# Kernel tuning notes

Measured on AMD Instinct MI355X. Metric: run time of the kernel, lower is better.

The kernel has to match this reference:

```python
import jax, jax.numpy as jnp
import numpy as np

N_NODES = 100000
N_EDGES = 1600000
IN_DIM = 300
HID = 128
N_CLASSES = 3
N_ASPECTS = 2048


def setup_inputs() -> dict:
    key = jax.random.key(0)
    ks = jax.random.split(key, 8)
    features = jax.random.normal(ks[0], (N_NODES, IN_DIM), dtype=jnp.float32)
    edge_index = jax.random.randint(ks[1], (2, N_EDGES), 0, N_NODES, dtype=jnp.int64)
    aspect_indices = jax.random.randint(ks[2], (N_ASPECTS,), 0, N_NODES, dtype=jnp.int64)
    W1 = jax.random.normal(ks[3], (IN_DIM, HID), dtype=jnp.float32) * (1.0 / np.sqrt(IN_DIM))
    b1 = jnp.zeros((HID,), dtype=jnp.float32)
    W2 = jax.random.normal(ks[4], (HID, HID), dtype=jnp.float32) * (1.0 / np.sqrt(HID))
    b2 = jnp.zeros((HID,), dtype=jnp.float32)
    Wc = jax.random.normal(ks[5], (HID, N_CLASSES), dtype=jnp.float32) * (1.0 / np.sqrt(HID))
    bc = jnp.zeros((N_CLASSES,), dtype=jnp.float32)
    return {"features": features, "edge_index": edge_index, "aspect_indices": aspect_indices,
            "W1": W1, "b1": b1, "W2": W2, "b2": b2, "Wc": Wc, "bc": bc}


def _gcn_norm(edge_index, num_nodes):
    # PyG GCNConv: add self-loops, symmetric normalization D^-1/2 (A+I) D^-1/2
    loop = jnp.arange(num_nodes, dtype=edge_index.dtype)
    src = jnp.concatenate([edge_index[0], loop])
    dst = jnp.concatenate([edge_index[1], loop])
    deg = jax.ops.segment_sum(jnp.ones_like(dst, dtype=jnp.float32), dst,
                              num_segments=num_nodes)
    deg_inv_sqrt = jnp.where(deg > 0, jax.lax.rsqrt(deg), 0.0)
    norm = deg_inv_sqrt[src] * deg_inv_sqrt[dst]  # [E + N]
    return src, dst, norm


def _gcn_conv(x, src, dst, norm, W, b, num_nodes):
    h = x @ W                            # transform first (dim reduction)
    msg = h[src] * norm[:, None]         # gather + scale  [E+N, HID]
    out = jax.ops.segment_sum(msg, dst, num_segments=num_nodes)  # scatter-add
    return out + b


def reference(features, edge_index, aspect_indices, W1, b1, W2, b2, Wc, bc):
    num_nodes = features.shape[0]
    src, dst, norm = _gcn_norm(edge_index, num_nodes)
    h = _gcn_conv(features, src, dst, norm, W1, b1, num_nodes)
    h = jax.nn.relu(h)
    # dropout(p=0.3) -> identity in eval mode
    h = _gcn_conv(h, src, dst, norm, W2, b2, num_nodes)
    aspect_embeddings = h[aspect_indices]          # [N_ASPECTS, HID]
    logits = aspect_embeddings @ Wc + bc           # [N_ASPECTS, 3]
    return logits
```

## Files before the change

kernel.cpp:

```cpp
#include <hip/hip_runtime.h>

constexpr int NN = 100000;
constexpr int NE = 1600000;
constexpr int IN_DIM = 300;
constexpr int HID = 128;
constexpr int NA = 2048;
constexpr int NF_CAP = 50000;
constexpr int G1_BLOCKS = 391;
constexpr int EDGE_BLOCKS = 782;

using short8 = __attribute__((ext_vector_type(8))) short;
using f32x4  = __attribute__((ext_vector_type(4))) float;

__device__ inline unsigned short f2bf(float x) {
    unsigned u = __float_as_uint(x);
    unsigned r = u + 0x7FFFu + ((u >> 16) & 1u);
    return (unsigned short)(r >> 16);
}
__device__ inline float bf2f(unsigned short h) {
    return __uint_as_float(((unsigned)h) << 16);
}

__device__ inline void gload_lds16(const void* g, void* l) {
    __builtin_amdgcn_global_load_lds(
        (const __attribute__((address_space(1))) unsigned int*)g,
        (__attribute__((address_space(3))) unsigned int*)l, 16, 0, 0);
}

__global__ void k_flag2(const int* __restrict__ asp, unsigned char* __restrict__ flags2,
                        int* __restrict__ flags1) {
    int i = blockIdx.x * blockDim.x + threadIdx.x;
    if (i < NA) {
        int n = asp[i];
        flags2[n] = 1;
        flags1[n] = 1;
    }
}

__global__ __launch_bounds__(1024) void k_scan2_local(const int* __restrict__ degi,
                                                      const int* __restrict__ flags1,
                                                      int* __restrict__ off,
                                                      int* __restrict__ off2,
                                                      int* __restrict__ blksum,
                                                      int* __restrict__ blksum2,
                                                      float* __restrict__ dis) {
    __shared__ int sh[1024];
    __shared__ int sh2[1024];
    int t = threadIdx.x;
    int base = blockIdx.x * 1024;
    int ok = (base + t < NN);
    int f = ok ? flags1[base + t] : 0;
    int d = ok ? degi[base + t] : 0;
    int v = f ? d : 0;
    if (ok) dis[base + t] = rsqrtf((float)d + 1.0f);
    sh[t] = v;
    sh2[t] = f;
    __syncthreads();
    for (int s = 1; s < 1024; s <<= 1) {
        int a = (t >= s) ? sh[t - s] : 0;
        int a2 = (t >= s) ? sh2[t - s] : 0;
        __syncthreads();
        sh[t] += a;
        sh2[t] += a2;
        __syncthreads();
    }
    if (ok) {
        off[base + t] = sh[t] - v;
        off2[base + t] = sh2[t] - f;
    }
    if (t == 1023) {
        blksum[blockIdx.x] = sh[1023];
        blksum2[blockIdx.x] = sh2[1023];
    }
}

__global__ __launch_bounds__(128) void k_scan2_blk(int* __restrict__ blksum,
                                                   int* __restrict__ blksum2, int nb) {
    __shared__ int sh[128];
    __shared__ int sh2[128];
    int t = threadIdx.x;
    int v = (t < nb) ? blksum[t] : 0;
    int v2 = (t < nb) ? blksum2[t] : 0;
    sh[t] = v;
    sh2[t] = v2;
    __syncthreads();
    for (int s = 1; s < 128; s <<= 1) {
        int a = (t >= s) ? sh[t - s] : 0;
        int a2 = (t >= s) ? sh2[t - s] : 0;
        __syncthreads();
        sh[t] += a;
        sh2[t] += a2;
        __syncthreads();
    }
    if (t < nb) {
        blksum[t] = sh[t] - v;
        blksum2[t] = sh2[t] - v2;
    }
}

__global__ void k_scan2_add(int* __restrict__ off, int* __restrict__ off2,
                            const int* __restrict__ blksum, const int* __restrict__ blksum2,
                            const int* __restrict__ flags1,
                            int* __restrict__ list, int* __restrict__ remap,
                            int* __restrict__ nf) {
    int i = blockIdx.x * blockDim.x + threadIdx.x;
    if (i < NN) {
        off[i] += blksum[i >> 10];
        int o2 = off2[i] + blksum2[i >> 10];
        off2[i] = o2;
        int f = flags1[i];
        if (f && o2 < NF_CAP) {
            list[o2] = i;
            remap[i] = o2;
        }
        if (i == NN - 1) {
            int tot = o2 + f;
            *nf = (tot < NF_CAP) ? tot : NF_CAP;
        }
    }
}

__global__ void k_prepB(const float* __restrict__ B, unsigned short* __restrict__ img,
                        int K, int NT) {
    int i = blockIdx.x * blockDim.x + threadIdx.x;
    if (i >= NT * 4096) return;
    int kt = i >> 12;
    int rem = i & 4095;
    int ct = rem >> 9;
    int s = rem & 511;
    int lg = s >> 7;
    int lr = (s >> 3) & 15;
    int j = s & 7;
    int k = kt * 32 + lg * 8 + j;
    int col = ct * 16 + lr;
    float v = (k < K) ? B[k * 128 + col] : 0.f;
    unsigned short hi = f2bf(v);
    unsigned short lo = f2bf(v - bf2f(hi));
    img[kt * 8192 + ct * 1024 + s] = hi;
    img[kt * 8192 + ct * 1024 + 512 + s] = lo;
}

template <int K, int NT>
__device__ __forceinline__ void gemm_dev(int gbid, const float* __restrict__ A,
        const unsigned short* __restrict__ Bimg,
        float* __restrict__ C, int M, const int* __restrict__ Mptr) {
    __shared__ alignas(16) unsigned short ldsB[2][8192];
    const int Mv = Mptr ? *Mptr : M;
    const int row0 = gbid * 128;
    if (row0 >= Mv) return;
    const int t = threadIdx.x;
    const int w = t >> 6;
    const int l = t & 63;
    const int lr = l & 15;
    const int lg = l >> 4;

    const int r0 = row0 + w * 16 + lr;
    const long a0 = (long)(r0 < Mv ? r0 : Mv - 1) * K + lg * 8;

    f32x4 acc[8];
#pragma unroll
    for (int ct = 0; ct < 8; ++ct) acc[ct] = (f32x4){0.f, 0.f, 0.f, 0.f};

    float4 A0[2], A1[2];

    auto LOADA = [&](float4* buf, int kt) {
        const int k0 = kt * 32 + lg * 8;
        const float* s0 = A + a0 + kt * 32;
        if (k0 + 8 <= K) {
            buf[0] = *(const float4*)(s0);
            buf[1] = *(const float4*)(s0 + 4);
        } else {
            float t0[8];
#pragma unroll
            for (int j = 0; j < 8; ++j) t0[j] = (k0 + j < K) ? s0[j] : 0.f;
            buf[0] = make_float4(t0[0], t0[1], t0[2], t0[3]);
            buf[1] = make_float4(t0[4], t0[5], t0[6], t0[7]);
        }
    };

    auto STAGE_B = [&](int buf, int kt) {
        const char* g = (const char*)Bimg + (long)kt * 16384 + w * 2048 + l * 16;
        gload_lds16(g, &ldsB[buf][w * 1024]);
        gload_lds16(g + 1024, &ldsB[buf][w * 1024 + 512]);
    };

    auto CONV = [&](const float4* buf, short8& h0, short8& e0) {
        float v0[8] = {buf[0].x, buf[0].y, buf[0].z, buf[0].w, buf[1].x, buf[1].y, buf[1].z, buf[1].w};
#pragma unroll
        for (int j = 0; j < 8; ++j) {
            unsigned short hi = f2bf(v0[j]);
            h0[j] = (short)hi;
            e0[j] = (short)f2bf(v0[j] - bf2f(hi));
        }
    };

    auto COMPUTE = [&](const unsigned short* bbuf, short8 ah, short8 al) {
#pragma unroll
        for (int ct = 0; ct < 8; ++ct) {
            const unsigned short* bp = bbuf + ct * 1024 + lg * 128 + lr * 8;
            short8 bh = *(const short8*)(bp);
            short8 bl = *(const short8*)(bp + 512);
            acc[ct] = __builtin_amdgcn_mfma_f32_16x16x32_bf16(ah, bh, acc[ct], 0, 0, 0);
            acc[ct] = __builtin_amdgcn_mfma_f32_16x16x32_bf16(al, bh, acc[ct], 0, 0, 0);
            acc[ct] = __builtin_amdgcn_mfma_f32_16x16x32_bf16(ah, bl, acc[ct], 0, 0, 0);
        }
    };

    LOADA(A0, 0);
    STAGE_B(0, 0);
    __syncthreads();
    for (int kt = 0; kt < NT; kt += 2) {
        if (kt + 1 < NT) {
            LOADA(A1, kt + 1);
            STAGE_B(1, kt + 1);
        }
        {
            short8 h0, e0;
            CONV(A0, h0, e0);
            COMPUTE(ldsB[0], h0, e0);
        }
        __syncthreads();
        if (kt + 1 < NT) {
            if (kt + 2 < NT) {
                LOADA(A0, kt + 2);
                STAGE_B(0, kt + 2);
            }
            short8 h0, e0;
            CONV(A1, h0, e0);
            COMPUTE(ldsB[1], h0, e0);
            __syncthreads();
        }
    }
#pragma unroll
    for (int ct = 0; ct < 8; ++ct)
#pragma unroll
        for (int r = 0; r < 4; ++r) {
            int row = row0 + w * 16 + lg * 4 + r;
            if (row < Mv) C[(long)row * 128 + ct * 16 + lr] = acc[ct][r];
        }
}

__global__ __launch_bounds__(512, 4) void k_fusedA(const float* __restrict__ A,
        const unsigned short* __restrict__ Bimg, float* __restrict__ C,
        const int* __restrict__ src, const int* __restrict__ dst,
        const unsigned char* __restrict__ flags2,
        int* __restrict__ degi, int* __restrict__ flags1) {
    if (blockIdx.x < G1_BLOCKS) {
        gemm_dev<IN_DIM, 10>(blockIdx.x, A, Bimg, C, NN, nullptr);
    } else {
        int e0 = (blockIdx.x - G1_BLOCKS) * 2048 + threadIdx.x * 4;
        if (e0 < NE) {
            int4 s4 = *(const int4*)(src + e0);
            int4 d4 = *(const int4*)(dst + e0);
            atomicAdd(&degi[d4.x], 1);
            atomicAdd(&degi[d4.y], 1);
            atomicAdd(&degi[d4.z], 1);
            atomicAdd(&degi[d4.w], 1);
            if (flags2[d4.x]) flags1[s4.x] = 1;
            if (flags2[d4.y]) flags1[s4.y] = 1;
            if (flags2[d4.z]) flags1[s4.z] = 1;
            if (flags2[d4.w]) flags1[s4.w] = 1;
        }
    }
}

__global__ __launch_bounds__(512, 4) void k_fusedB(const float* __restrict__ A,
        const unsigned short* __restrict__ Bimg, float* __restrict__ C,
        const int* __restrict__ src, const int* __restrict__ dst,
        const int* __restrict__ flags1,
        int* __restrict__ off, int* __restrict__ csr) {
    if (blockIdx.x < G1_BLOCKS) {
        gemm_dev<IN_DIM, 10>(blockIdx.x + G1_BLOCKS, A, Bimg, C, NN, nullptr);
    } else {
        int e0 = (blockIdx.x - G1_BLOCKS) * 2048 + threadIdx.x * 4;
        if (e0 < NE) {
            int4 s4 = *(const int4*)(src + e0);
            int4 d4 = *(const int4*)(dst + e0);
            if (flags1[d4.x]) csr[atomicAdd(&off[d4.x], 1)] = s4.x;
            if (flags1[d4.y]) csr[atomicAdd(&off[d4.y], 1)] = s4.y;
            if (flags1[d4.z]) csr[atomicAdd(&off[d4.z], 1)] = s4.z;
            if (flags1[d4.w]) csr[atomicAdd(&off[d4.w], 1)] = s4.w;
        }
    }
}

__global__ __launch_bounds__(512, 4) void k_gemm2(const float* __restrict__ A,
        const unsigned short* __restrict__ Bimg, float* __restrict__ C,
        const int* __restrict__ nf) {
    gemm_dev<HID, 4>(blockIdx.x, A, Bimg, C, 0, nf);
}

__global__ __launch_bounds__(256) void k_gather1(const int* __restrict__ list,
                                                 const int* __restrict__ nf,
                                                 const int* __restrict__ csr,
                                                 const int* __restrict__ offpost,
                                                 const float* __restrict__ dis,
                                                 const float* __restrict__ h1,
                                                 const float* __restrict__ b1,
                                                 float* __restrict__ out) {
    int wave = threadIdx.x >> 6;
    int lane = threadIdx.x & 63;
    int half = lane >> 5;
    int sl = lane & 31;
    int idx = blockIdx.x * 4 + wave;
    if (idx >= *nf) return;
    int n = list[idx];
    int start = (n == 0) ? 0 : offpost[n - 1];
    int end = offpost[n];
    float dn = dis[n];
    float ax = 0.f, ay = 0.f, az = 0.f, aw = 0.f;
    int i = start + half;
    for (; i + 2 < end; i += 4) {
        int s0 = csr[i], s1 = csr[i + 2];
        float w0 = dis[s0], w1 = dis[s1];
        float4 v0 = *(const float4*)&h1[(long)s0 * HID + sl * 4];
        float4 v1 = *(const float4*)&h1[(long)s1 * HID + sl * 4];
        ax += w0 * v0.x + w1 * v1.x;
        ay += w0 * v0.y + w1 * v1.y;
        az += w0 * v0.z + w1 * v1.z;
        aw += w0 * v0.w + w1 * v1.w;
    }
    if (i < end) {
        int s = csr[i];
        float wgt = dis[s];
        float4 v = *(const float4*)&h1[(long)s * HID + sl * 4];
        ax += wgt * v.x;
        ay += wgt * v.y;
        az += wgt * v.z;
        aw += wgt * v.w;
    }
    ax += __shfl_xor(ax, 32);
    ay += __shfl_xor(ay, 32);
    az += __shfl_xor(az, 32);
    aw += __shfl_xor(aw, 32);
    if (half == 0) {
        float4 hv = *(const float4*)&h1[(long)n * HID + sl * 4];
        float4 bv = *(const float4*)&b1[sl * 4];
        float4 r;
        r.x = fmaxf(dn * (ax + dn * hv.x) + bv.x, 0.f);
        r.y = fmaxf(dn * (ay + dn * hv.y) + bv.y, 0.f);
        r.z = fmaxf(dn * (az + dn * hv.z) + bv.z, 0.f);
        r.w = fmaxf(dn * (aw + dn * hv.w) + bv.w, 0.f);
        *reinterpret_cast<float4*>(&out[(long)idx * HID + sl * 4]) = r;
    }
}

__global__ __launch_bounds__(256) void k_gather2(const int* __restrict__ asp,
                                                 const int* __restrict__ remap,
                                                 const int* __restrict__ csr,
                                                 const int* __restrict__ offpost,
                                                 const float* __restrict__ dis,
                                                 const float* __restrict__ t2,
                                                 const float* __restrict__ b2,
                                                 const float* __restrict__ Wc,
                                                 const float* __restrict__ bc,
                                                 float* __restrict__ out) {
    int wave = threadIdx.x >> 6;
    int lane = threadIdx.x & 63;
    int a = blockIdx.x * 4 + wave;
    if (a >= NA) return;
    int n = asp[a];
    int start = (n == 0) ? 0 : offpost[n - 1];
    int end = offpost[n];
    float dn = dis[n];
    float ax = 0.f, ay = 0.f;
    int i = start;
    for (; i + 4 <= end; i += 4) {
        int s0 = csr[i], s1 = csr[i + 1], s2 = csr[i + 2], s3 = csr[i + 3];
        float w0 = dis[s0], w1 = dis[s1], w2 = dis[s2], w3 = dis[s3];
        int r0 = remap[s0], r1 = remap[s1], r2 = remap[s2], r3 = remap[s3];
        float2 v0 = *(const float2*)&t2[(long)r0 * HID + lane * 2];
        float2 v1 = *(const float2*)&t2[(long)r1 * HID + lane * 2];
        float2 v2 = *(const float2*)&t2[(long)r2 * HID + lane * 2];
        float2 v3 = *(const float2*)&t2[(long)r3 * HID + lane * 2];
        ax += w0 * v0.x + w1 * v1.x + w2 * v2.x + w3 * v3.x;
        ay += w0 * v0.y + w1 * v1.y + w2 * v2.y + w3 * v3.y;
    }
    for (; i < end; ++i) {
        int s = csr[i];
        float w = dis[s];
        float2 v = *(const float2*)&t2[(long)remap[s] * HID + lane * 2];
        ax += w * v.x;
        ay += w * v.y;
    }
    float2 hv = *(const float2*)&t2[(long)remap[n] * HID + lane * 2];
    float vx = dn * (ax + dn * hv.x) + b2[2 * lane];
    float vy = dn * (ay + dn * hv.y) + b2[2 * lane + 1];
    float l0 = vx * Wc[(2 * lane) * 3 + 0] + vy * Wc[(2 * lane + 1) * 3 + 0];
    float l1 = vx * Wc[(2 * lane) * 3 + 1] + vy * Wc[(2 * lane + 1) * 3 + 1];
    float l2 = vx * Wc[(2 * lane) * 3 + 2] + vy * Wc[(2 * lane + 1) * 3 + 2];
#pragma unroll
    for (int s = 32; s > 0; s >>= 1) {
        l0 += __shfl_xor(l0, s);
        l1 += __shfl_xor(l1, s);
        l2 += __shfl_xor(l2, s);
    }
    if (lane == 0) {
        out[a * 3 + 0] = l0 + bc[0];
        out[a * 3 + 1] = l1 + bc[1];
        out[a * 3 + 2] = l2 + bc[2];
    }
}

extern "C" void kernel_launch(void* const* d_in, const int* in_sizes, int n_in,
                              void* d_out, int out_size, void* d_ws, size_t ws_size,
                              hipStream_t stream) {
    const float* features = (const float*)d_in[0];
    const int* ei = (const int*)d_in[1];
    const int* src = ei;
    const int* dst = ei + NE;
    const int* asp = (const int*)d_in[2];
    const float* W1 = (const float*)d_in[3];
    const float* b1 = (const float*)d_in[4];
    const float* W2 = (const float*)d_in[5];
    const float* b2 = (const float*)d_in[6];
    const float* Wc = (const float*)d_in[7];
    const float* bc = (const float*)d_in[8];
    float* out = (float*)d_out;

    char* ws = (char*)d_ws;
    float* dis   = (float*)(ws + 0);
    unsigned short* bimg1 = (unsigned short*)(ws + 400384);
    unsigned short* bimg2 = (unsigned short*)(ws + 400384 + 163840);
    int*   off   = (int*)  (ws + 800768);
    int*   blksum  = (int*)(ws + 1201152);
    int*   blksum2 = (int*)(ws + 1202176);
    int*   nf    = (int*)  (ws + 1203200);
    int*   csr   = (int*)  (ws + 1203328);
    int*   flags1= (int*)  (ws + 7603328);
    int*   off2  = (int*)  (ws + 8003328);
    int*   list  = (int*)  (ws + 8403328);
    int*   remap = (int*)  (ws + 8803328);
    float* bufA  = (float*)(ws + 9203328);
    float* bufB  = (float*)(ws + 60403328);
    int*   degi  = (int*)  (ws + 60403328);
    unsigned char* flags2 = (unsigned char*)(ws + 86003328);

    const int NB = (NN + 1023) / 1024;

    hipMemsetAsync(degi, 0, NN * sizeof(int), stream);
    hipMemsetAsync(flags1, 0, NN * sizeof(int), stream);
    hipMemsetAsync(flags2, 0, NN, stream);
    k_flag2<<<(NA + 255) / 256, 256, 0, stream>>>(asp, flags2, flags1);
    k_prepB<<<(10 * 4096 + 255) / 256, 256, 0, stream>>>(W1, bimg1, IN_DIM, 10);
    k_prepB<<<(4 * 4096 + 255) / 256, 256, 0, stream>>>(W2, bimg2, HID, 4);

    k_fusedA<<<G1_BLOCKS + EDGE_BLOCKS, 512, 0, stream>>>(
        features, bimg1, bufA, src, dst, flags2, degi, flags1);

    k_scan2_local<<<NB, 1024, 0, stream>>>(degi, flags1, off, off2, blksum, blksum2, dis);
    k_scan2_blk<<<1, 128, 0, stream>>>(blksum, blksum2, NB);
    k_scan2_add<<<(NN + 255) / 256, 256, 0, stream>>>(off, off2, blksum, blksum2,
                                                      flags1, list, remap, nf);

    k_fusedB<<<G1_BLOCKS + EDGE_BLOCKS, 512, 0, stream>>>(
        features, bimg1, bufA, src, dst, flags1, off, csr);

    k_gather1<<<(NF_CAP + 3) / 4, 256, 0, stream>>>(list, nf, csr, off, dis, bufA, b1, bufB);

    k_gemm2<<<(NF_CAP + 127) / 128, 512, 0, stream>>>(bufB, bimg2, bufA, nf);
    k_gather2<<<(NA + 3) / 4, 256, 0, stream>>>(asp, remap, csr, off, dis, bufA, b2, Wc, bc, out);
}
```

Baseline: 201.4 us.

## Restructure GEMM to 64-row tiles with 3-stage LDS pipeline for A and B

The GEMM tile shrinks from 128 to 64 rows, and 8 waves now split as 4 row groups by 2 column halves. The A operand is staged into LDS via global_load_lds with an XOR swizzle instead of register loads. A triple-buffered LDS ring with explicit vmcnt waits and raw s_barrier overlaps loads two k-steps ahead. This roughly doubles block counts for both GEMMs, aiming for better latency hiding and load balance. The cost is more LDS per block (72KB), which may reduce occupancy, plus more redundant B staging.

```diff
diff --git a/kernel.cpp b/kernel.cpp
--- a/kernel.cpp
+++ b/kernel.cpp
@@ -6,7 +6,9 @@
 constexpr int HID = 128;
 constexpr int NA = 2048;
 constexpr int NF_CAP = 50000;
-constexpr int G1_BLOCKS = 391;
+constexpr int G1T = 1563;
+constexpr int G1A = 782;
+constexpr int G1B = G1T - G1A;
 constexpr int EDGE_BLOCKS = 782;
 
 using short8 = __attribute__((ext_vector_type(8))) short;
@@ -144,99 +146,88 @@
 __device__ __forceinline__ void gemm_dev(int gbid, const float* __restrict__ A,
         const unsigned short* __restrict__ Bimg,
         float* __restrict__ C, int M, const int* __restrict__ Mptr) {
-    __shared__ alignas(16) unsigned short ldsB[2][8192];
+    __shared__ alignas(16) char lds[3][24576];
     const int Mv = Mptr ? *Mptr : M;
-    const int row0 = gbid * 128;
+    const int row0 = gbid * 64;
     if (row0 >= Mv) return;
     const int t = threadIdx.x;
     const int w = t >> 6;
     const int l = t & 63;
     const int lr = l & 15;
     const int lg = l >> 4;
-
-    const int r0 = row0 + w * 16 + lr;
-    const long a0 = (long)(r0 < Mv ? r0 : Mv - 1) * K + lg * 8;
-
-    f32x4 acc[8];
-#pragma unroll
-    for (int ct = 0; ct < 8; ++ct) acc[ct] = (f32x4){0.f, 0.f, 0.f, 0.f};
-
-    float4 A0[2], A1[2];
-
-    auto LOADA = [&](float4* buf, int kt) {
-        const int k0 = kt * 32 + lg * 8;
-        const float* s0 = A + a0 + kt * 32;
-        if (k0 + 8 <= K) {
-            buf[0] = *(const float4*)(s0);
-            buf[1] = *(const float4*)(s0 + 4);
-        } else {
-            float t0[8];
-#pragma unroll
-            for (int j = 0; j < 8; ++j) t0[j] = (k0 + j < K) ? s0[j] : 0.f;
-            buf[0] = make_float4(t0[0], t0[1], t0[2], t0[3]);
-            buf[1] = make_float4(t0[4], t0[5], t0[6], t0[7]);
-        }
+    const int wr = w & 3;
+    const int wc = w >> 2;
+
+    const int srow_loc = w * 8 + (l >> 3);
+    const int srow = row0 + srow_loc;
+    const long arow = (long)(srow < Mv ? srow : Mv - 1) * K;
+    const int schunk = (l & 7) ^ ((l >> 3) & 7);
+
+    f32x4 acc[4];
+#pragma unroll
+    for (int ct = 0; ct < 4; ++ct) acc[ct] = (f32x4){0.f, 0.f, 0.f, 0.f};
+
+    auto STAGE = [&](int buf, int kt) {
+        const char* gb = (const char*)Bimg + (long)kt * 16384 + w * 2048 + l * 16;
+        gload_lds16(gb,        lds[buf] + w * 2048);
+        gload_lds16(gb + 1024, lds[buf] + w * 2048 + 1024);
+        int kk = kt * 32 + schunk * 4;
+        if (kk > K - 4) kk = K - 4;
+        const float* ga = A + arow + kk;
+        gload_lds16(ga, lds[buf] + 16384 + w * 1024);
     };
 
-    auto STAGE_B = [&](int buf, int kt) {
-        const char* g = (const char*)Bimg + (long)kt * 16384 + w * 2048 + l * 16;
-        gload_lds16(g, &ldsB[buf][w * 1024]);
-        gload_lds16(g + 1024, &ldsB[buf][w * 1024 + 512]);
-    };
-
-    auto CONV = [&](const float4* buf, short8& h0, short8& e0) {
-        float v0[8] = {buf[0].x, buf[0].y, buf[0].z, buf[0].w, buf[1].x, buf[1].y, buf[1].z, buf[1].w};
-#pragma unroll
-        for (int j = 0; j < 8; ++j) {
-            unsigned short hi = f2bf(v0[j]);
-            h0[j] = (short)hi;
-            e0[j] = (short)f2bf(v0[j] - bf2f(hi));
-        }
-    };
-
-    auto COMPUTE = [&](const unsigned short* bbuf, short8 ah, short8 al) {
-#pragma unroll
-        for (int ct = 0; ct < 8; ++ct) {
-            const unsigned short* bp = bbuf + ct * 1024 + lg * 128 + lr * 8;
-            short8 bh = *(const short8*)(bp);
-            short8 bl = *(const short8*)(bp + 512);
-            acc[ct] = __builtin_amdgcn_mfma_f32_16x16x32_bf16(ah, bh, acc[ct], 0, 0, 0);
-            acc[ct] = __builtin_amdgcn_mfma_f32_16x16x32_bf16(al, bh, acc[ct], 0, 0, 0);
-            acc[ct] = __builtin_amdgcn_mfma_f32_16x16x32_bf16(ah, bl, acc[ct], 0, 0, 0);
-        }
-    };
-
-    LOADA(A0, 0);
-    STAGE_B(0, 0);
-    __syncthreads();
-    for (int kt = 0; kt < NT; kt += 2) {
+    STAGE(0, 0);
+    STAGE(1, 1);
+    asm volatile("s_waitcnt vmcnt(3)" ::: "memory");
+    __builtin_amdgcn_sched_barrier(0);
+    __builtin_amdgcn_s_barrier();
+    __builtin_amdgcn_sched_barrier(0);
+
+#pragma unroll
+    for (int kt = 0; kt < NT; ++kt) {
+        if (kt + 2 < NT) STAGE((kt + 2) % 3, kt + 2);
+        {
+            const char* ab = lds[kt % 3] + 16384;
+            const int rbyte = (wr * 16 + lr) * 128;
+            float4 f0 = *(const float4*)(ab + rbyte + (((lg * 2 + 0) ^ (lr & 7)) << 4));
+            float4 f1 = *(const float4*)(ab + rbyte + (((lg * 2 + 1) ^ (lr & 7)) << 4));
+            float av[8] = {f0.x, f0.y, f0.z, f0.w, f1.x, f1.y, f1.z, f1.w};
+            short8 ah, al;
+#pragma unroll
+            for (int j = 0; j < 8; ++j) {
+                unsigned short hi = f2bf(av[j]);
+                ah[j] = (short)hi;
+                al[j] = (short)f2bf(av[j] - bf2f(hi));
+            }
+            const unsigned short* bb = (const unsigned short*)lds[kt % 3];
+#pragma unroll
+            for (int ct = 0; ct < 4; ++ct) {
+                const unsigned short* bp = bb + (wc * 4 + ct) * 1024 + lg * 128 + lr * 8;
+                short8 bh = *(const short8*)(bp);
+                short8 bl = *(const short8*)(bp + 512);
+                acc[ct] = __builtin_amdgcn_mfma_f32_16x16x32_bf16(ah, bh, acc[ct], 0, 0, 0);
+                acc[ct] = __builtin_amdgcn_mfma_f32_16x16x32_bf16(al, bh, acc[ct], 0, 0, 0);
+                acc[ct] = __builtin_amdgcn_mfma_f32_16x16x32_bf16(ah, bl, acc[ct], 0, 0, 0);
+            }
+        }
+        __builtin_amdgcn_sched_barrier(0);
+        if (kt + 2 < NT) {
+            asm volatile("s_waitcnt vmcnt(3)" ::: "memory");
+        } else if (kt + 1 < NT) {
+            asm volatile("s_waitcnt vmcnt(0)" ::: "memory");
+        }
         if (kt + 1 < NT) {
-            LOADA(A1, kt + 1);
-            STAGE_B(1, kt + 1);
-        }
-        {
-            short8 h0, e0;
-            CONV(A0, h0, e0);
-            COMPUTE(ldsB[0], h0, e0);
-        }
-        __syncthreads();
-        if (kt + 1 < NT) {
-            if (kt + 2 < NT) {
-                LOADA(A0, kt + 2);
-                STAGE_B(0, kt + 2);
-            }
-            short8 h0, e0;
-            CONV(A1, h0, e0);
-            COMPUTE(ldsB[1], h0, e0);
-            __syncthreads();
-        }
-    }
-#pragma unroll
-    for (int ct = 0; ct < 8; ++ct)
+            __builtin_amdgcn_s_barrier();
+            __builtin_amdgcn_sched_barrier(0);
+        }
+    }
+#pragma unroll
+    for (int ct = 0; ct < 4; ++ct)
 #pragma unroll
         for (int r = 0; r < 4; ++r) {
-            int row = row0 + w * 16 + lg * 4 + r;
-            if (row < Mv) C[(long)row * 128 + ct * 16 + lr] = acc[ct][r];
+            int row = row0 + wr * 16 + lg * 4 + r;
+            if (row < Mv) C[(long)row * 128 + wc * 64 + ct * 16 + lr] = acc[ct][r];
         }
 }
 
@@ -245,10 +236,10 @@
         const int* __restrict__ src, const int* __restrict__ dst,
         const unsigned char* __restrict__ flags2,
         int* __restrict__ degi, int* __restrict__ flags1) {
-    if (blockIdx.x < G1_BLOCKS) {
+    if (blockIdx.x < G1A) {
         gemm_dev<IN_DIM, 10>(blockIdx.x, A, Bimg, C, NN, nullptr);
     } else {
-        int e0 = (blockIdx.x - G1_BLOCKS) * 2048 + threadIdx.x * 4;
+        int e0 = (blockIdx.x - G1A) * 2048 + threadIdx.x * 4;
         if (e0 < NE) {
             int4 s4 = *(const int4*)(src + e0);
             int4 d4 = *(const int4*)(dst + e0);
@@ -269,10 +260,10 @@
         const int* __restrict__ src, const int* __restrict__ dst,
         const int* __restrict__ flags1,
         int* __restrict__ off, int* __restrict__ csr) {
-    if (blockIdx.x < G1_BLOCKS) {
-        gemm_dev<IN_DIM, 10>(blockIdx.x + G1_BLOCKS, A, Bimg, C, NN, nullptr);
+    if (blockIdx.x < G1B) {
+        gemm_dev<IN_DIM, 10>(blockIdx.x + G1A, A, Bimg, C, NN, nullptr);
     } else {
-        int e0 = (blockIdx.x - G1_BLOCKS) * 2048 + threadIdx.x * 4;
+        int e0 = (blockIdx.x - G1B) * 2048 + threadIdx.x * 4;
         if (e0 < NE) {
             int4 s4 = *(const int4*)(src + e0);
             int4 d4 = *(const int4*)(dst + e0);
@@ -445,7 +436,7 @@
     k_prepB<<<(10 * 4096 + 255) / 256, 256, 0, stream>>>(W1, bimg1, IN_DIM, 10);
     k_prepB<<<(4 * 4096 + 255) / 256, 256, 0, stream>>>(W2, bimg2, HID, 4);
 
-    k_fusedA<<<G1_BLOCKS + EDGE_BLOCKS, 512, 0, stream>>>(
+    k_fusedA<<<G1A + EDGE_BLOCKS, 512, 0, stream>>>(
         features, bimg1, bufA, src, dst, flags2, degi, flags1);
 
     k_scan2_local<<<NB, 1024, 0, stream>>>(degi, flags1, off, off2, blksum, blksum2, dis);
@@ -453,11 +444,11 @@
     k_scan2_add<<<(NN + 255) / 256, 256, 0, stream>>>(off, off2, blksum, blksum2,
                                                       flags1, list, remap, nf);
 
-    k_fusedB<<<G1_BLOCKS + EDGE_BLOCKS, 512, 0, stream>>>(
+    k_fusedB<<<G1B + EDGE_BLOCKS, 512, 0, stream>>>(
         features, bimg1, bufA, src, dst, flags1, off, csr);
 
     k_gather1<<<(NF_CAP + 3) / 4, 256, 0, stream>>>(list, nf, csr, off, dis, bufA, b1, bufB);
 
-    k_gemm2<<<(NF_CAP + 127) / 128, 512, 0, stream>>>(bufB, bimg2, bufA, nf);
+    k_gemm2<<<(NF_CAP + 63) / 64, 512, 0, stream>>>(bufB, bimg2, bufA, nf);
     k_gather2<<<(NA + 3) / 4, 256, 0, stream>>>(asp, remap, csr, off, dis, bufA, b2, Wc, bc, out);
 }
```

New measurement: 212.2 us. 1.05x slower.
